# Kernel optimization log

Measured on AMD Instinct MI355X. Metric: run time of the kernel, lower is better.

Reference implementation:

```python
import jax, jax.numpy as jnp
import numpy as np

B, C, N = 8, 128, 4096
C2 = C // 2
BN_EPS = 1e-5


def setup_inputs() -> dict:
    key = jax.random.key(0)
    ks = jax.random.split(key, 8)
    s = 1.0 / np.sqrt(C)
    s2 = 1.0 / np.sqrt(C2)
    return {
        "x": jax.random.normal(ks[0], (B, C, N), dtype=jnp.float32),
        "w_qk": jax.random.uniform(ks[1], (C2, C), jnp.float32, -s, s),  # shared q/k weight
        "w_v": jax.random.uniform(ks[2], (C2, C), jnp.float32, -s, s),
        "b_v": jax.random.uniform(ks[3], (C2,), jnp.float32, -s, s),
        "w_x": jax.random.uniform(ks[4], (C2, C), jnp.float32, -s, s),
        "w_t": jax.random.uniform(ks[5], (C2, C2), jnp.float32, -s2, s2),
        "b_t": jax.random.uniform(ks[6], (C2,), jnp.float32, -s2, s2),
        "gamma": jnp.ones((C2,), jnp.float32),
        "beta": jnp.zeros((C2,), jnp.float32),
    }


def reference(x, w_qk, w_v, b_v, w_x, w_t, b_t, gamma, beta):
    # 1x1 convs are per-point linear maps: [B,C,N] -> [B,C2,N]
    x_q = jnp.einsum("oc,bcn->bno", w_qk, x)          # [B, N, C2]
    x_k = jnp.einsum("oc,bcn->bon", w_qk, x)          # [B, C2, N]
    x_v = jnp.einsum("oc,bcn->bon", w_v, x) + b_v[None, :, None]

    energy = jnp.einsum("bno,bom->bnm", x_q, x_k)     # [B, N, N]
    attn = jax.nn.softmax(energy, axis=-1)            # row softmax
    attn = attn / (1e-9 + attn.sum(axis=1, keepdims=True))  # column L1 renorm

    x_r = jnp.einsum("bon,bnm->bom", x_v, attn)       # [B, C2, N]
    x_c = jnp.einsum("oc,bcn->bon", w_x, x)           # [B, C2, N]

    d = x_c - x_r
    t = jnp.einsum("oi,bin->bon", w_t, d) + b_t[None, :, None]
    # BatchNorm1d (training-mode batch stats) over (B, N) per channel
    mean = t.mean(axis=(0, 2), keepdims=True)
    var = t.var(axis=(0, 2), keepdims=True)
    t_hat = (t - mean) * jax.lax.rsqrt(var + BN_EPS)
    x_r2 = jax.nn.relu(gamma[None, :, None] * t_hat + beta[None, :, None])
    return x_c + x_r2
```

## Files before the change

kernel.cpp:

```cpp
#include <hip/hip_runtime.h>

#define B_   8
#define C_   128
#define N_   4096
#define C2_  64

typedef __bf16 bf16x8 __attribute__((ext_vector_type(8)));
typedef float  f32x4  __attribute__((ext_vector_type(4)));

#define MFMA16(a, b, c) __builtin_amdgcn_mfma_f32_16x16x32_bf16((a), (b), (c), 0, 0, 0)

#define QK_SCALE 1.2011224087864498f

static __device__ __forceinline__ unsigned short f2bf(float f) {
    union { __bf16 b; unsigned short u; } cv;
    cv.b = (__bf16)f;
    return cv.u;
}
static __device__ __forceinline__ float bf2f(unsigned short u) {
    union { unsigned int u; float f; } cv;
    cv.u = ((unsigned int)u) << 16;
    return cv.f;
}

struct us4 { unsigned short a, b, c, d; };

static __device__ __forceinline__ void gl_lds16(const unsigned short* g, void* l) {
    __builtin_amdgcn_global_load_lds(
        (const __attribute__((address_space(1))) unsigned int*)g,
        (__attribute__((address_space(3))) unsigned int*)l,
        16, 0, 0);
}

__global__ __launch_bounds__(256) void k0_wcvt(
    const float* __restrict__ wq, const float* __restrict__ wv,
    const float* __restrict__ wx, unsigned short* __restrict__ wst)
{
    const int i4 = (blockIdx.x * 256 + threadIdx.x) * 4;
    const int mat = i4 >> 13;
    const float* src = (mat == 0) ? wq : (mat == 1) ? wv : wx;
    const float sc = (mat == 0) ? QK_SCALE : 1.0f;
    const float4 v = *(const float4*)(src + (i4 & 8191));
    us4 pk;
    pk.a = f2bf(v.x * sc); pk.b = f2bf(v.y * sc);
    pk.c = f2bf(v.z * sc); pk.d = f2bf(v.w * sc);
    *(us4*)(wst + i4) = pk;
}

__global__ __launch_bounds__(256) void k1_proj(
    const float* __restrict__ x, const unsigned short* __restrict__ wst,
    const float* __restrict__ b_v,
    unsigned short* __restrict__ qk_t, unsigned short* __restrict__ xv_bf,
    unsigned short* __restrict__ xc_bf)
{
    __shared__ __align__(16) unsigned short w_lds[192 * 128];
    __shared__ __align__(16) unsigned short x_t[64 * 136];
    const int tid = threadIdx.x;
    const int wave = tid >> 6, lane = tid & 63;
    const int quad = lane >> 4, col = lane & 15;
    const int b = blockIdx.y;
    const int n0 = blockIdx.x * 64;

    #pragma unroll
    for (int it = 0; it < 12; ++it) {
        const int idx = it * 256 + tid;
        const int row = idx >> 4, seg = idx & 15;
        gl_lds16(wst + (size_t)row * 128 + (size_t)(seg ^ (row & 7)) * 8,
                 w_lds + idx * 8);
    }
    const float* xb = x + (size_t)b * C_ * N_ + n0;
    #pragma unroll
    for (int it = 0; it < 8; ++it) {
        const int idx = it * 256 + tid;
        const int c = idx >> 4, n = (idx & 15) * 4;
        const float4 v = *(const float4*)(xb + (size_t)c * N_ + n);
        x_t[(n + 0) * 136 + c] = f2bf(v.x);
        x_t[(n + 1) * 136 + c] = f2bf(v.y);
        x_t[(n + 2) * 136 + c] = f2bf(v.z);
        x_t[(n + 3) * 136 + c] = f2bf(v.w);
    }
    __syncthreads();

    const int nw = wave * 16;
    bf16x8 bfr[4];
    #pragma unroll
    for (int kt = 0; kt < 4; ++kt)
        bfr[kt] = *(const bf16x8*)&x_t[(nw + col) * 136 + kt * 32 + quad * 8];

    const int n_g = n0 + nw + col;

    #pragma unroll
    for (int ot = 0; ot < 12; ++ot) {
        f32x4 acc = {0.f, 0.f, 0.f, 0.f};
        #pragma unroll
        for (int kt = 0; kt < 4; ++kt) {
            const bf16x8 afr = *(const bf16x8*)&w_lds[
                ((ot * 16 + col) << 7) + (((kt * 4 + quad) ^ (col & 7)) << 3)];
            acc = MFMA16(afr, bfr[kt], acc);
        }
        if (ot < 4) {
            us4 pk;
            pk.a = f2bf(acc[0]); pk.b = f2bf(acc[1]);
            pk.c = f2bf(acc[2]); pk.d = f2bf(acc[3]);
            *(us4*)&qk_t[(size_t)(b * N_ + n_g) * C2_ + ot * 16 + quad * 4] = pk;
        } else if (ot < 8) {
            const float4 bv4 = *(const float4*)(b_v + (ot - 4) * 16 + quad * 4);
            const float* bvp = (const float*)&bv4;
            #pragma unroll
            for (int r = 0; r < 4; ++r)
                xv_bf[(size_t)(b * C2_ + (ot - 4) * 16 + quad * 4 + r) * N_ + n_g]
                    = f2bf(acc[r] + bvp[r]);
        } else {
            #pragma unroll
            for (int r = 0; r < 4; ++r)
                xc_bf[(size_t)(b * C2_ + (ot - 8) * 16 + quad * 4 + r) * N_ + n_g]
                    = f2bf(acc[r]);
        }
    }
}

__global__ __launch_bounds__(256) void k2_sym(
    const unsigned short* __restrict__ qk_t, float* __restrict__ part_rs)
{
    __shared__ __align__(16) unsigned short slab[128 * 64];
    __shared__ float cwl[4 * 128];
    const int tid = threadIdx.x;
    const int wave = tid >> 6, lane = tid & 63;
    const int quad = lane >> 4, col = lane & 15;
    const int b = blockIdx.x & 7;
    int job = blockIdx.x >> 3, ti = 0;
    while (job >= 32 - ti) { job -= 32 - ti; ++ti; }
    const int tj = ti + job;
    const unsigned short* qb = qk_t + (size_t)b * N_ * C2_;

    const int n_base = ti * 128 + wave * 32;
    bf16x8 a0[2], a1[2];
    #pragma unroll
    for (int s = 0; s < 2; ++s) {
        const unsigned short* p = qb + (size_t)(n_base + s * 16 + col) * C2_ + quad * 8;
        a0[s] = *(const bf16x8*)p;
        a1[s] = *(const bf16x8*)(p + 32);
    }

    #pragma unroll
    for (int r = 0; r < 4; ++r) {
        const int idx = r * 256 + tid;
        const int row = idx >> 3, seg = idx & 7;
        gl_lds16(qb + (size_t)(tj * 128 + row) * C2_ + (size_t)(seg ^ (row & 7)) * 8,
                 slab + idx * 8);
    }
    __syncthreads();

    float run_s[2][4];
    #pragma unroll
    for (int s = 0; s < 2; ++s)
        #pragma unroll
        for (int r = 0; r < 4; ++r) run_s[s][r] = 0.f;

    #pragma unroll
    for (int g = 0; g < 8; ++g) {
        const int row = g * 16 + col;
        const bf16x8 b0 = *(const bf16x8*)(slab + row * 64 + ((quad ^ (col & 7)) * 8));
        const bf16x8 b1 = *(const bf16x8*)(slab + row * 64 + (((4 + quad) ^ (col & 7)) * 8));
        float cs = 0.f;
        #pragma unroll
        for (int s = 0; s < 2; ++s) {
            f32x4 acc = {0.f, 0.f, 0.f, 0.f};
            __builtin_amdgcn_s_setprio(1);
            acc = MFMA16(a0[s], b0, acc);
            acc = MFMA16(a1[s], b1, acc);
            __builtin_amdgcn_s_setprio(0);
            #pragma unroll
            for (int r = 0; r < 4; ++r) {
                const float u = __builtin_amdgcn_exp2f(acc[r]);
                run_s[s][r] += u;
                cs += u;
            }
        }
        cs += __shfl_xor(cs, 16, 64);
        cs += __shfl_xor(cs, 32, 64);
        if (quad == 0) cwl[wave * 128 + g * 16 + col] = cs;
    }
    __syncthreads();
    if (ti != tj && tid < 128) {
        const float c = cwl[tid] + cwl[128 + tid] + cwl[256 + tid] + cwl[384 + tid];
        part_rs[((size_t)(ti * 8 + b) << 12) + tj * 128 + tid] = c;
    }

    #pragma unroll
    for (int s = 0; s < 2; ++s)
        #pragma unroll
        for (int r = 0; r < 4; ++r) {
            #pragma unroll
            for (int off = 1; off < 16; off <<= 1)
                run_s[s][r] += __shfl_xor(run_s[s][r], off, 64);
        }
    if (col == 0) {
        #pragma unroll
        for (int s = 0; s < 2; ++s)
            #pragma unroll
            for (int r = 0; r < 4; ++r)
                part_rs[((size_t)(tj * 8 + b) << 12) + n_base + s * 16 + quad * 4 + r]
                    = run_s[s][r];
    }
}

__global__ __launch_bounds__(64) void k2w(
    const float* __restrict__ part_rs, float* __restrict__ lw)
{
    const int b = blockIdx.x & 7;
    const int n = (blockIdx.x >> 3) * 64 + threadIdx.x;
    float s = 0.f;
    #pragma unroll
    for (int t = 0; t < 32; ++t)
        s += part_rs[((size_t)(t * 8 + b) << 12) + n];
    lw[b * N_ + n] = -__log2f(s);
}

__global__ __launch_bounds__(512, 4) void k3_pv(
    const unsigned short* __restrict__ qk_t, const unsigned short* __restrict__ xv_bf,
    const float* __restrict__ lw,
    unsigned short* __restrict__ yb0, unsigned short* __restrict__ yb1,
    float* __restrict__ cspart)
{
    __shared__ __align__(16) unsigned char lds_raw[32768 + 8 * 2560];
    const int tid = threadIdx.x;
    const int wave = tid >> 6, lane = tid & 63;
    const int quad = lane >> 4, col = lane & 15;
    const int nh2 = wave & 1, mh = wave >> 1;
    const int b = blockIdx.x & 7;
    const int m_blk = ((blockIdx.x >> 3) & 31) * 128;
    const int sk = blockIdx.x >> 8;
    const int n_start = sk * 2048;
    const int n_chunks = 32;
    const int m_wave = m_blk + mh * 32;
    const unsigned short* qb = qk_t + (size_t)b * N_ * C2_;
    const unsigned short* vb = xv_bf + (size_t)b * C2_ * N_;
    const float* ln = lw + b * N_;
    unsigned short* yp = (sk == 0) ? yb0 : yb1;

    bf16x8 kb0[2], kb1[2];
    #pragma unroll
    for (int g = 0; g < 2; ++g) {
        const unsigned short* p = qb + (size_t)(m_wave + g * 16 + col) * C2_ + quad * 8;
        kb0[g] = *(const bf16x8*)p;
        kb1[g] = *(const bf16x8*)(p + 32);
    }

    bf16x8 ones;
    #pragma unroll
    for (int j = 0; j < 8; ++j) ones[j] = (__bf16)1.0f;

    unsigned short* stS = (unsigned short*)(lds_raw + 32768 + wave * 2560);

    auto stage = [&](int n0, int p) {
        unsigned char* qbase = lds_raw + p * 8192;
        unsigned char* vbase = lds_raw + 16384 + p * 8192;
        const int row = tid >> 3, seg = tid & 7;
        const int ss = seg ^ (row & 7);
        gl_lds16(qb + (size_t)(n0 + row) * C2_ + (size_t)ss * 8, qbase + tid * 16);
        gl_lds16(vb + (size_t)row * N_ + n0 + ss * 8, vbase + tid * 16);
    };

    f32x4 accY[2][4];
    #pragma unroll
    for (int g = 0; g < 2; ++g)
        #pragma unroll
        for (int os = 0; os < 4; ++os) accY[g][os] = (f32x4){0.f, 0.f, 0.f, 0.f};
    f32x4 csacc[2];
    #pragma unroll
    for (int g = 0; g < 2; ++g) csacc[g] = (f32x4){0.f, 0.f, 0.f, 0.f};

    const float* lwp = ln + n_start + nh2 * 32 + quad * 4;
    float4 lwA = *(const float4*)(lwp);
    float4 lwB = *(const float4*)(lwp + 16);

    stage(n_start, 0);
    __syncthreads();

    for (int c = 0; c < n_chunks; ++c) {
        const int n0 = n_start + c * 64;
        const int p = c & 1;
        if (c + 1 < n_chunks) stage(n0 + 64, 1 - p);

        const unsigned short* qt = (const unsigned short*)(lds_raw + p * 8192);
        const unsigned short* vt = (const unsigned short*)(lds_raw + 16384 + p * 8192);

        #pragma unroll
        for (int ns = 0; ns < 2; ++ns) {
            const int row = nh2 * 32 + ns * 16 + col;
            const bf16x8 qa0 = *(const bf16x8*)(qt + row * 64 + ((quad ^ (col & 7)) * 8));
            const bf16x8 qa1 = *(const bf16x8*)(qt + row * 64 + (((4 + quad) ^ (col & 7)) * 8));
            const float4 lw4 = ns ? lwB : lwA;
            #pragma unroll
            for (int g = 0; g < 2; ++g) {
                f32x4 acc = {lw4.x, lw4.y, lw4.z, lw4.w};
                acc = MFMA16(qa0, kb0[g], acc);
                acc = MFMA16(qa1, kb1[g], acc);
                union { unsigned short us[4]; uint2 u2; } pk;
                #pragma unroll
                for (int r = 0; r < 4; ++r)
                    pk.us[r] = f2bf(__builtin_amdgcn_exp2f(acc[r]));
                *(uint2*)&stS[(g * 16 + col) * 40 + ns * 16 + quad * 4] = pk.u2;
            }
        }

        if (c + 1 < n_chunks) {
            lwA = *(const float4*)(lwp + (c + 1) * 64);
            lwB = *(const float4*)(lwp + (c + 1) * 64 + 16);
        }

        bf16x8 sB[2];
        #pragma unroll
        for (int g = 0; g < 2; ++g)
            sB[g] = *(const bf16x8*)&stS[(g * 16 + col) * 40 + quad * 8];

        #pragma unroll
        for (int g = 0; g < 2; ++g)
            csacc[g] = MFMA16(ones, sB[g], csacc[g]);

        #pragma unroll
        for (int os = 0; os < 4; ++os) {
            const bf16x8 va = *(const bf16x8*)(vt + (os * 16 + col) * 64 +
                                               (((nh2 * 4 + quad) ^ (col & 7)) * 8));
            #pragma unroll
            for (int g = 0; g < 2; ++g)
                accY[g][os] = MFMA16(va, sB[g], accY[g][os]);
        }
        __syncthreads();
    }

    float* cmb = (float*)lds_raw;
    float* csc = (float*)(lds_raw + 32768);
    if (nh2 == 1) {
        #pragma unroll
        for (int g = 0; g < 2; ++g) {
            #pragma unroll
            for (int os = 0; os < 4; ++os)
                #pragma unroll
                for (int r = 0; r < 4; ++r)
                    cmb[((mh * 8 + g * 4 + os) * 4 + r) * 64 + lane] = accY[g][os][r];
            csc[(mh * 2 + g) * 64 + lane] = csacc[g][0];
        }
    }
    __syncthreads();
    if (nh2 == 0) {
        #pragma unroll
        for (int g = 0; g < 2; ++g) {
            const float cs = csacc[g][0] + csc[(mh * 2 + g) * 64 + lane];
            if (lane < 16)
                cspart[((size_t)sk * 8 + b) * N_ + m_wave + g * 16 + lane] = cs;
            #pragma unroll
            for (int os = 0; os < 4; ++os)
                #pragma unroll
                for (int r = 0; r < 4; ++r) {
                    const float v = accY[g][os][r] +
                        cmb[((mh * 8 + g * 4 + os) * 4 + r) * 64 + lane];
                    yp[(size_t)(b * C2_ + os * 16 + quad * 4 + r) * N_ + m_wave + g * 16 + col]
                        = f2bf(v);
                }
        }
    }
}

__global__ __launch_bounds__(256) void k4_t(
    const unsigned short* __restrict__ xc_bf, const unsigned short* __restrict__ y0,
    const unsigned short* __restrict__ y1,
    const float* __restrict__ cspart, const float* __restrict__ w_t,
    const float* __restrict__ b_t, unsigned short* __restrict__ t_bf,
    float* __restrict__ part_bn)
{
    __shared__ __align__(16) unsigned short wlds[64 * 72];
    __shared__ __align__(16) unsigned short d_t[64 * 72];
    __shared__ float cinv[64];
    const int tid = threadIdx.x;
    const int wave = tid >> 6, lane = tid & 63;
    const int quad = lane >> 4, col = lane & 15;
    const int b = blockIdx.y;
    const int n0 = blockIdx.x * 64;
    const size_t base = (size_t)b * C2_ * N_;

    #pragma unroll
    for (int it = 0; it < 4; ++it) {
        const int idx4 = it * 256 + tid;
        const int o = idx4 >> 4, i4 = (idx4 & 15) * 4;
        const float4 v = *(const float4*)(w_t + o * 64 + i4);
        us4 pk;
        pk.a = f2bf(v.x); pk.b = f2bf(v.y); pk.c = f2bf(v.z); pk.d = f2bf(v.w);
        *(us4*)&wlds[o * 72 + i4] = pk;
    }
    if (tid < 64) {
        const int n = n0 + tid;
        const float cs = cspart[(size_t)b * N_ + n] + cspart[(size_t)(8 + b) * N_ + n];
        cinv[tid] = 1.0f / (1e-9f + cs);
    }
    __syncthreads();

    #pragma unroll
    for (int it = 0; it < 4; ++it) {
        const int idx4 = it * 256 + tid;
        const int i = idx4 >> 4, n4 = (idx4 & 15) * 4;
        const size_t g = base + (size_t)i * N_ + n0 + n4;
        const us4 cx = *(const us4*)(xc_bf + g);
        const us4 u0 = *(const us4*)(y0 + g);
        const us4 u1 = *(const us4*)(y1 + g);
        d_t[(n4 + 0) * 72 + i] = f2bf(bf2f(cx.a) - (bf2f(u0.a) + bf2f(u1.a)) * cinv[n4 + 0]);
        d_t[(n4 + 1) * 72 + i] = f2bf(bf2f(cx.b) - (bf2f(u0.b) + bf2f(u1.b)) * cinv[n4 + 1]);
        d_t[(n4 + 2) * 72 + i] = f2bf(bf2f(cx.c) - (bf2f(u0.c) + bf2f(u1.c)) * cinv[n4 + 2]);
        d_t[(n4 + 3) * 72 + i] = f2bf(bf2f(cx.d) - (bf2f(u0.d) + bf2f(u1.d)) * cinv[n4 + 3]);
    }
    __syncthreads();

    const int ow = wave * 16;
    bf16x8 afr[2];
    #pragma unroll
    for (int kt = 0; kt < 2; ++kt)
        afr[kt] = *(const bf16x8*)&wlds[(ow + col) * 72 + kt * 32 + quad * 8];
    const float4 bt4 = *(const float4*)(b_t + ow + quad * 4);
    const float* btp = (const float*)&bt4;

    float s[4] = {0.f, 0.f, 0.f, 0.f}, q2[4] = {0.f, 0.f, 0.f, 0.f};
    #pragma unroll
    for (int ns = 0; ns < 4; ++ns) {
        f32x4 acc = {0.f, 0.f, 0.f, 0.f};
        #pragma unroll
        for (int kt = 0; kt < 2; ++kt) {
            const bf16x8 bfr = *(const bf16x8*)&d_t[(ns * 16 + col) * 72 + kt * 32 + quad * 8];
            acc = MFMA16(afr[kt], bfr, acc);
        }
        #pragma unroll
        for (int r = 0; r < 4; ++r) {
            const float t = acc[r] + btp[r];
            t_bf[base + (size_t)(ow + quad * 4 + r) * N_ + n0 + ns * 16 + col] = f2bf(t);
            s[r] += t;
            q2[r] += t * t;
        }
    }
    #pragma unroll
    for (int r = 0; r < 4; ++r) {
        #pragma unroll
        for (int off = 1; off < 16; off <<= 1) {
            s[r]  += __shfl_xor(s[r],  off, 64);
            q2[r] += __shfl_xor(q2[r], off, 64);
        }
    }
    if (col == 0) {
        const int blk = blockIdx.x * 8 + b;
        #pragma unroll
        for (int r = 0; r < 4; ++r) {
            part_bn[(size_t)(ow + quad * 4 + r) * 512 + blk]      = s[r];
            part_bn[(size_t)(64 + ow + quad * 4 + r) * 512 + blk] = q2[r];
        }
    }
}

__global__ __launch_bounds__(256) void k5r(
    const float* __restrict__ part_bn, float* __restrict__ bn)
{
    const int c = blockIdx.x;
    const int tid = threadIdx.x, wave = tid >> 6, lane = tid & 63;
    float s = 0.f;
    for (int j = tid; j < 512; j += 256) s += part_bn[(size_t)c * 512 + j];
    #pragma unroll
    for (int off = 1; off < 64; off <<= 1) s += __shfl_xor(s, off, 64);
    __shared__ float red[4];
    if (lane == 0) red[wave] = s;
    __syncthreads();
    if (tid == 0) bn[c] = red[0] + red[1] + red[2] + red[3];
}

__global__ __launch_bounds__(256) void k6_out(
    const unsigned short* __restrict__ xc_bf, const unsigned short* __restrict__ t_bf,
    const float* __restrict__ bn, const float* __restrict__ gamma,
    const float* __restrict__ beta, float* __restrict__ out)
{
    const int idx = blockIdx.x * 256 + threadIdx.x;
    const int o = (idx >> 10) & 63;
    const float invC = 1.0f / (float)(B_ * N_);
    const float mean = bn[o] * invC;
    const float var  = bn[64 + o] * invC - mean * mean;
    const float sc = gamma[o] * rsqrtf(var + 1e-5f);
    const float sh = beta[o] - mean * sc;
    const us4 t4 = ((const us4*)t_bf)[idx];
    const us4 c4 = ((const us4*)xc_bf)[idx];
    float4 r;
    r.x = bf2f(c4.a) + fmaxf(0.f, sc * bf2f(t4.a) + sh);
    r.y = bf2f(c4.b) + fmaxf(0.f, sc * bf2f(t4.b) + sh);
    r.z = bf2f(c4.c) + fmaxf(0.f, sc * bf2f(t4.c) + sh);
    r.w = bf2f(c4.d) + fmaxf(0.f, sc * bf2f(t4.d) + sh);
    ((float4*)out)[idx] = r;
}

extern "C" void kernel_launch(void* const* d_in, const int* in_sizes, int n_in,
                              void* d_out, int out_size, void* d_ws, size_t ws_size,
                              hipStream_t stream) {
    const float* x     = (const float*)d_in[0];
    const float* w_qk  = (const float*)d_in[1];
    const float* w_v   = (const float*)d_in[2];
    const float* b_v   = (const float*)d_in[3];
    const float* w_x   = (const float*)d_in[4];
    const float* w_t   = (const float*)d_in[5];
    const float* b_t   = (const float*)d_in[6];
    const float* gamma = (const float*)d_in[7];
    const float* beta  = (const float*)d_in[8];
    float* out = (float*)d_out;

    char* ws = (char*)d_ws;
    unsigned short* qk_t  = (unsigned short*)ws;
    unsigned short* xv_bf = (unsigned short*)(ws + (4  << 20));
    unsigned short* xc_bf = (unsigned short*)(ws + (8  << 20));
    unsigned short* t_bf  = (unsigned short*)(ws + (12 << 20));
    unsigned short* yb0 = (unsigned short*)(ws + (16 << 20));
    unsigned short* yb1 = (unsigned short*)(ws + (20 << 20));
    float* part_rs = (float*)(ws + (24 << 20));
    float* cspart  = (float*)(ws + (32 << 20));
    float* part_bn = (float*)(ws + (33 << 20));
    float* bn      = (float*)(ws + (33 << 20) + (256 << 10));
    unsigned short* wstack = (unsigned short*)d_out;
    float* lw = (float*)((char*)d_out + (256 << 10));

    hipLaunchKernelGGL(k0_wcvt,     dim3(24),     256, 0, stream, w_qk, w_v, w_x, wstack);
    hipLaunchKernelGGL(k1_proj,     dim3(64, 8),  256, 0, stream,
                       x, wstack, b_v, qk_t, xv_bf, xc_bf);
    hipLaunchKernelGGL(k2_sym,      dim3(4224),   256, 0, stream, qk_t, part_rs);
    hipLaunchKernelGGL(k2w,         dim3(512),    64,  0, stream, part_rs, lw);
    hipLaunchKernelGGL(k3_pv,       dim3(512),    512, 0, stream,
                       qk_t, xv_bf, lw, yb0, yb1, cspart);
    hipLaunchKernelGGL(k4_t,        dim3(64, 8),  256, 0, stream,
                       xc_bf, yb0, yb1, cspart, w_t, b_t, t_bf, part_bn);
    hipLaunchKernelGGL(k5r,         dim3(128),    256, 0, stream, part_bn, bn);
    hipLaunchKernelGGL(k6_out,      dim3(2048),   256, 0, stream, xc_bf, t_bf, bn, gamma, beta, out);
}
```

Baseline: 163.6 us.

## Replace BN reduction kernel with atomics, pad S staging stride, widen k2w blocks

```diff
diff --git a/kernel.cpp b/kernel.cpp
--- a/kernel.cpp
+++ b/kernel.cpp
@@ -34,8 +34,10 @@
 
 __global__ __launch_bounds__(256) void k0_wcvt(
     const float* __restrict__ wq, const float* __restrict__ wv,
-    const float* __restrict__ wx, unsigned short* __restrict__ wst)
-{
+    const float* __restrict__ wx, unsigned short* __restrict__ wst,
+    float* __restrict__ bn)
+{
+    if (blockIdx.x == 0 && threadIdx.x < 128) bn[threadIdx.x] = 0.f;
     const int i4 = (blockIdx.x * 256 + threadIdx.x) * 4;
     const int mat = i4 >> 13;
     const float* src = (mat == 0) ? wq : (mat == 1) ? wv : wx;
@@ -205,11 +207,11 @@
     }
 }
 
-__global__ __launch_bounds__(64) void k2w(
+__global__ __launch_bounds__(256) void k2w(
     const float* __restrict__ part_rs, float* __restrict__ lw)
 {
-    const int b = blockIdx.x & 7;
-    const int n = (blockIdx.x >> 3) * 64 + threadIdx.x;
+    const int idx = blockIdx.x * 256 + threadIdx.x;
+    const int b = idx >> 12, n = idx & 4095;
     float s = 0.f;
     #pragma unroll
     for (int t = 0; t < 32; ++t)
@@ -223,7 +225,7 @@
     unsigned short* __restrict__ yb0, unsigned short* __restrict__ yb1,
     float* __restrict__ cspart)
 {
-    __shared__ __align__(16) unsigned char lds_raw[32768 + 8 * 2560];
+    __shared__ __align__(16) unsigned char lds_raw[32768 + 8 * 2688];
     const int tid = threadIdx.x;
     const int wave = tid >> 6, lane = tid & 63;
     const int quad = lane >> 4, col = lane & 15;
@@ -251,7 +253,7 @@
     #pragma unroll
     for (int j = 0; j < 8; ++j) ones[j] = (__bf16)1.0f;
 
-    unsigned short* stS = (unsigned short*)(lds_raw + 32768 + wave * 2560);
+    unsigned short* stS = (unsigned short*)(lds_raw + 32768 + wave * 2688);
 
     auto stage = [&](int n0, int p) {
         unsigned char* qbase = lds_raw + p * 8192;
@@ -301,7 +303,7 @@
                 #pragma unroll
                 for (int r = 0; r < 4; ++r)
                     pk.us[r] = f2bf(__builtin_amdgcn_exp2f(acc[r]));
-                *(uint2*)&stS[(g * 16 + col) * 40 + ns * 16 + quad * 4] = pk.u2;
+                *(uint2*)&stS[(g * 16 + col) * 42 + ns * 16 + quad * 4] = pk.u2;
             }
         }
 
@@ -313,7 +315,7 @@
         bf16x8 sB[2];
         #pragma unroll
         for (int g = 0; g < 2; ++g)
-            sB[g] = *(const bf16x8*)&stS[(g * 16 + col) * 40 + quad * 8];
+            sB[g] = *(const bf16x8*)&stS[(g * 16 + col) * 42 + quad * 8];
 
         #pragma unroll
         for (int g = 0; g < 2; ++g)
@@ -368,7 +370,7 @@
     const unsigned short* __restrict__ y1,
     const float* __restrict__ cspart, const float* __restrict__ w_t,
     const float* __restrict__ b_t, unsigned short* __restrict__ t_bf,
-    float* __restrict__ part_bn)
+    float* __restrict__ bn)
 {
     __shared__ __align__(16) unsigned short wlds[64 * 72];
     __shared__ __align__(16) unsigned short d_t[64 * 72];
@@ -445,28 +447,12 @@
         }
     }
     if (col == 0) {
-        const int blk = blockIdx.x * 8 + b;
         #pragma unroll
         for (int r = 0; r < 4; ++r) {
-            part_bn[(size_t)(ow + quad * 4 + r) * 512 + blk]      = s[r];
-            part_bn[(size_t)(64 + ow + quad * 4 + r) * 512 + blk] = q2[r];
-        }
-    }
-}
-
-__global__ __launch_bounds__(256) void k5r(
-    const float* __restrict__ part_bn, float* __restrict__ bn)
-{
-    const int c = blockIdx.x;
-    const int tid = threadIdx.x, wave = tid >> 6, lane = tid & 63;
-    float s = 0.f;
-    for (int j = tid; j < 512; j += 256) s += part_bn[(size_t)c * 512 + j];
-    #pragma unroll
-    for (int off = 1; off < 64; off <<= 1) s += __shfl_xor(s, off, 64);
-    __shared__ float red[4];
-    if (lane == 0) red[wave] = s;
-    __syncthreads();
-    if (tid == 0) bn[c] = red[0] + red[1] + red[2] + red[3];
+            atomicAdd(&bn[ow + quad * 4 + r], s[r]);
+            atomicAdd(&bn[64 + ow + quad * 4 + r], q2[r]);
+        }
+    }
 }
 
 __global__ __launch_bounds__(256) void k6_out(
@@ -514,20 +500,18 @@
     unsigned short* yb1 = (unsigned short*)(ws + (20 << 20));
     float* part_rs = (float*)(ws + (24 << 20));
     float* cspart  = (float*)(ws + (32 << 20));
-    float* part_bn = (float*)(ws + (33 << 20));
-    float* bn      = (float*)(ws + (33 << 20) + (256 << 10));
+    float* bn      = (float*)(ws + (33 << 20));
     unsigned short* wstack = (unsigned short*)d_out;
     float* lw = (float*)((char*)d_out + (256 << 10));
 
-    hipLaunchKernelGGL(k0_wcvt,     dim3(24),     256, 0, stream, w_qk, w_v, w_x, wstack);
+    hipLaunchKernelGGL(k0_wcvt,     dim3(24),     256, 0, stream, w_qk, w_v, w_x, wstack, bn);
     hipLaunchKernelGGL(k1_proj,     dim3(64, 8),  256, 0, stream,
                        x, wstack, b_v, qk_t, xv_bf, xc_bf);
     hipLaunchKernelGGL(k2_sym,      dim3(4224),   256, 0, stream, qk_t, part_rs);
-    hipLaunchKernelGGL(k2w,         dim3(512),    64,  0, stream, part_rs, lw);
+    hipLaunchKernelGGL(k2w,         dim3(128),    256, 0, stream, part_rs, lw);
     hipLaunchKernelGGL(k3_pv,       dim3(512),    512, 0, stream,
                        qk_t, xv_bf, lw, yb0, yb1, cspart);
     hipLaunchKernelGGL(k4_t,        dim3(64, 8),  256, 0, stream,
-                       xc_bf, yb0, yb1, cspart, w_t, b_t, t_bf, part_bn);
-    hipLaunchKernelGGL(k5r,         dim3(128),    256, 0, stream, part_bn, bn);
+                       xc_bf, yb0, yb1, cspart, w_t, b_t, t_bf, bn);
     hipLaunchKernelGGL(k6_out,      dim3(2048),   256, 0, stream, xc_bf, t_bf, bn, gamma, beta, out);
 }
```

Result: slower. 282.4 us (+72.7%).
